# Kernel tuning notes

Measured on AMD Instinct MI355X. Metric: run time of the kernel, lower is better.

The kernel has to match this reference:

```python
import jax, jax.numpy as jnp
import numpy as np

D_FEAT = 64          # d
N_CTX = 8192         # n
N_LAYERS = 4         # l
LMBD = 0.9
DIM = 2 * D_FEAT + 1 # 129


def _decay_matrix(n, lmbd, dtype):
    # M[i, j] = lmbd**(i-j) for j <= i <= n-1 (lower-triangular geometric decay);
    # last row (and hence M[n, n]) is zero, matching the torch loop construction.
    idx = jnp.arange(n + 1)
    diff = idx[:, None] - idx[None, :]
    M = jnp.where(diff >= 0,
                  jnp.power(jnp.asarray(lmbd, dtype), jnp.maximum(diff, 0).astype(dtype)),
                  jnp.zeros((), dtype))
    return M.at[n].set(0.0)


def setup_inputs() -> dict:
    key = jax.random.key(0)
    kz, kp, kq = jax.random.split(key, 3)
    # xavier_normal with gain 0.1 on square (DIM, DIM) weights:
    std = 0.1 * np.sqrt(2.0 / (DIM + DIM))
    Z = jax.random.normal(kz, (DIM, N_CTX + 1), dtype=jnp.float32)
    P = std * jax.random.normal(kp, (DIM, DIM), dtype=jnp.float32)
    Q = std * jax.random.normal(kq, (DIM, DIM), dtype=jnp.float32)
    return {"Z": Z, "P": P, "Q": Q}


def reference(Z, P, Q):
    n = Z.shape[1] - 1
    M = _decay_matrix(n, LMBD, Z.dtype)
    inv_n = jnp.asarray(1.0 / n, Z.dtype)

    def attn(Zc):
        # X = Z^T Q Z : (n+1, n+1)
        X = Zc.T @ Q @ Zc
        A = jax.nn.softmax(X, axis=-1)        # activation('softmax')
        # left-to-right as in torch: ((P @ Z) @ M) @ A, each (DIM, n+1)
        return Zc + inv_n * (((P @ Zc) @ M) @ A)

    for _ in range(N_LAYERS):  # mode='auto': same layer applied l times
        Z = attn(Z)
    return Z
```

## Files before the change

### kernel.cpp

```cpp
#include <hip/hip_runtime.h>

#define D 129
#define N1 8193
#define NN 8192
#define INV_N (1.0f/8192.0f)
#define WSTR 8448
#define KP 160
#define TROWS 8448
#define PSTR 8320

typedef __attribute__((ext_vector_type(8))) short bf16x8;
typedef __attribute__((ext_vector_type(4))) float f32x4;
typedef __attribute__((ext_vector_type(4))) unsigned u32x4;
typedef __attribute__((ext_vector_type(2))) unsigned u32x2;

__device__ __forceinline__ short f2bf(float x){
  unsigned u = __float_as_uint(x);
  unsigned r = (u + 0x7fffu + ((u>>16)&1u)) >> 16;
  return (short)r;
}

__device__ __forceinline__ unsigned cvtpk(float a, float b){
  unsigned r; asm("v_cvt_pk_bf16_f32 %0, %1, %2" : "=v"(r) : "v"(a), "v"(b)); return r;
}

__device__ __forceinline__ float bf2f(unsigned short v){
  return __uint_as_float(((unsigned)v)<<16);
}

#define GLOAD_LDS16(gp, lp) __builtin_amdgcn_global_load_lds( \
    (const __attribute__((address_space(1))) void*)(gp),      \
    (__attribute__((address_space(3))) void*)(lp), 16, 0, 0)

__device__ __forceinline__ int tau(int pos){
  return (pos & 96) + ((pos & 4) << 2) + ((pos & 24) >> 1) + (pos & 3);
}

__global__ void k_tr(const float* __restrict__ src, short* __restrict__ dst, int tmax){
  __shared__ float tile[129][65];
  int t0 = blockIdx.x*64, tid = threadIdx.x;
  for(int idx=tid; idx<129*64; idx+=256){
    int d = idx>>6, c = idx&63;
    tile[d][c] = (t0+c < tmax)? src[(size_t)d*N1 + t0+c] : 0.f;
  }
  __syncthreads();
  int q = tid&3, tl = tid>>2;
  int t = t0 + tl;
  short* row = dst + (size_t)t*KP;
  int s7 = t&7;
  #pragma unroll
  for(int g5=0; g5<5; g5++){
    int gi = q*5 + g5;
    bf16x8 v;
    if(gi < 16){
      #pragma unroll
      for(int u=0;u<8;u++) v[u] = f2bf(tile[gi*8+u][tl]);
      *(bf16x8*)(row + ((gi^s7)<<3)) = v;
    } else if(gi == 16){
      v[0] = f2bf(tile[128][tl]);
      #pragma unroll
      for(int u=1;u<8;u++) v[u] = 0;
      *(bf16x8*)(row + (16<<3)) = v;
    } else {
      #pragma unroll
      for(int u=0;u<8;u++) v[u] = 0;
      *(bf16x8*)(row + (gi<<3)) = v;
    }
  }
}

__global__ __launch_bounds__(512) void k_small(
    const float* __restrict__ Z, const float* __restrict__ P,
    const float* __restrict__ Q, short* __restrict__ YT,
    float* __restrict__ PZ){
  __shared__ float qs[8][132], ps[8][132];
  __shared__ float red[16*256];
  const int tid = threadIdx.x, tx = tid&255, kg = tid>>8;
  const int r0 = blockIdx.y*8;
  for(int i=tid;i<8*129;i+=512){
    int rr=i/129, cc=i-rr*129;
    float qv=0.f, pv=0.f;
    if(r0+rr<D){ qv=Q[(r0+rr)*D+cc]; pv=P[(r0+rr)*D+cc]; }
    qs[rr][cc]=qv; ps[rr][cc]=pv;
  }
  __syncthreads();
  const int t = blockIdx.x*256 + tx;
  const bool valid = (t < N1);
  const int tc = valid ? t : (N1-1);
  const float* zp = Z + tc;
  float ay[8], ap[8];
  #pragma unroll
  for(int rr=0;rr<8;rr++){ ay[rr]=0.f; ap[rr]=0.f; }
  const int kbeg = kg ? 65 : 0, kend = kg ? 129 : 65;
  for(int k=kbeg;k<kend;k++){
    float z = zp[(size_t)k*N1];
    #pragma unroll
    for(int rr=0;rr<8;rr++){
      ay[rr] = fmaf(qs[rr][k], z, ay[rr]);
      ap[rr] = fmaf(ps[rr][k], z, ap[rr]);
    }
  }
  if(kg==1){
    #pragma unroll
    for(int rr=0;rr<8;rr++){
      red[rr*256+tx]     = ay[rr];
      red[(8+rr)*256+tx] = ap[rr];
    }
  }
  __syncthreads();
  if(kg==0){
    #pragma unroll
    for(int rr=0;rr<8;rr++){
      ay[rr] += red[rr*256+tx];
      ap[rr] += red[(8+rr)*256+tx];
    }
    short* row = YT + (size_t)t*KP;
    const int s7 = t&7;
    const int gc = r0>>3;
    bf16x8 v;
    #pragma unroll
    for(int u=0;u<8;u++) v[u] = f2bf(valid ? ay[u] : 0.f);
    if(gc < 16){
      *(bf16x8*)(row + ((gc^s7)<<3)) = v;
    } else {
      *(bf16x8*)(row + (16<<3)) = v;
      bf16x8 zv;
      #pragma unroll
      for(int u=0;u<8;u++) zv[u]=0;
      *(bf16x8*)(row + (17<<3)) = zv;
      *(bf16x8*)(row + (18<<3)) = zv;
      *(bf16x8*)(row + (19<<3)) = zv;
    }
    #pragma unroll
    for(int rr=0;rr<8;rr++){
      int r=r0+rr;
      if(r<D) PZ[(size_t)r*WSTR + t] = valid ? ap[rr] : 0.f;
    }
  }
}

__global__ void k_scan(const float* __restrict__ PZ, float* __restrict__ W){
  __shared__ float s[2376];
  int d = blockIdx.y;
  int base = blockIdx.x*2048;
  for(int i=threadIdx.x;i<2304;i+=128){
    int j = base+i;
    s[i + (i>>5)] = (j<NN)? PZ[(size_t)d*WSTR + j] : 0.f;
  }
  __syncthreads();
  int t = threadIdx.x;
  int jh = t*16+15;
  float acc = 0.f, f = 1.f;
  for(int k=0;k<256;k++){ int a = jh+k; acc = fmaf(f, s[a+(a>>5)], acc); f *= 0.9f; }
  float wv[16];
  wv[15] = acc;
  #pragma unroll
  for(int r=14;r>=0;r--){ int a = t*16+r; wv[r] = fmaf(0.9f, wv[r+1], s[a+(a>>5)]); }
  float* out = W + (size_t)d*WSTR + base + t*16;
  #pragma unroll
  for(int r=0;r<16;r+=4) *(f32x4*)(out+r) = (f32x4){wv[r],wv[r+1],wv[r+2],wv[r+3]};
}

__global__ void k_ssum(const float* __restrict__ S_part, float* __restrict__ S,
                       int i_base, int count){
  int idx = blockIdx.x*256+threadIdx.x;
  if(idx>=count) return;
  int i = i_base + idx;
  float s=0.f;
  #pragma unroll 3
  for(int jtb=0;jtb<33;jtb++) s += S_part[(size_t)jtb*WSTR + i];
  S[i]=s;
}

__global__ void k_v(const float* __restrict__ W, const float* __restrict__ S,
                    short* __restrict__ Vt, int tile0){
  int idx = blockIdx.x*256+threadIdx.x;
  int l = idx/18432, rem = idx - l*18432;
  int d = rem>>7, ci = rem&127;
  int it = tile0 + l;
  int i = it*128 + tau(ci);
  float v = (d<=128)? W[(size_t)d*WSTR + i]/S[i] : 0.f;
  int gs = (ci>>3) ^ (d&7);
  Vt[(size_t)it*18432 + (d<<7) + gs*8 + (ci&7)] = f2bf(v);
}

__global__ __launch_bounds__(512,4) void k_qke(
    const short* __restrict__ ZT, const short* __restrict__ YT,
    short* __restrict__ Ebuf, float* __restrict__ S_part, int tile0, int ITC, int nwg){
  __shared__ short zt[128*KP];
  __shared__ short sp[32*132];
  const int tid=threadIdx.x, w=tid>>6, lane=tid&63, g=lane>>4, lm=lane&15;
  int bid = blockIdx.x;
  int qq = nwg>>3, rr8 = nwg&7, xcd = bid&7, ix = bid>>3;
  int wg = (xcd<rr8 ? xcd*(qq+1) : rr8*(qq+1)+(xcd-rr8)*qq) + ix;
  const int jtb = wg/ITC, itl = wg - jtb*ITC;
  const int it = tile0 + itl;
  const int sx = lm&7;

  const short* ztg = ZT + (size_t)it*(128*KP);
  #pragma unroll
  for(int q=0;q<5;q++){
    int off = (q*512 + tid)*8;
    GLOAD_LDS16(ztg + off, zt + off);
  }

  bf16x8 b[2][5];
  #pragma unroll
  for(int p=0;p<2;p++){
    int jr = jtb*256 + w*32 + p*16 + lm;
    const short* rp = YT + (size_t)jr*KP;
    #pragma unroll
    for(int kk=0;kk<4;kk++) b[p][kk] = *(const bf16x8*)(rp + (((kk*4+g)^sx)<<3));
    b[p][4] = *(const bf16x8*)(rp + ((16+g)<<3));
  }
  const int jl0 = w*32 + lm, jl1 = jl0 + 16;
  const bool jv0 = (jtb*256 + jl0) < N1;
  const bool jv1 = (jtb*256 + jl1) < N1;
  short* ep0 = Ebuf + ((size_t)(jtb*2 + (jl0>>7))*ITC + itl)*16384 + (jl0&127)*128;
  short* ep1 = Ebuf + ((size_t)(jtb*2 + (jl1>>7))*ITC + itl)*16384 + (jl1&127)*128;
  const int wl = w*4 + (lm>>2);
  __syncthreads();

  #pragma unroll
  for(int p2=0;p2<4;p2++){
    const int ib0 = 2*p2, ib1 = ib0+1;
    f32x4 aA0={0.f,0.f,0.f,0.f}, aA1={0.f,0.f,0.f,0.f};
    f32x4 aB0={0.f,0.f,0.f,0.f}, aB1={0.f,0.f,0.f,0.f};
    const short* zpA = zt + (ib0*16+lm)*KP;
    const short* zpB = zt + (ib1*16+lm)*KP;
    #pragma unroll
    for(int kk=0;kk<4;kk++){
      bf16x8 fa = *(const bf16x8*)(zpA + (((kk*4+g)^sx)<<3));
      bf16x8 fb = *(const bf16x8*)(zpB + (((kk*4+g)^sx)<<3));
      aA0 = __builtin_amdgcn_mfma_f32_16x16x32_bf16(fa, b[0][kk], aA0, 0,0,0);
      aA1 = __builtin_amdgcn_mfma_f32_16x16x32_bf16(fa, b[1][kk], aA1, 0,0,0);
      aB0 = __builtin_amdgcn_mfma_f32_16x16x32_bf16(fb, b[0][kk], aB0, 0,0,0);
      aB1 = __builtin_amdgcn_mfma_f32_16x16x32_bf16(fb, b[1][kk], aB1, 0,0,0);
    }
    {
      bf16x8 fa = *(const bf16x8*)(zpA + ((16+g)<<3));
      bf16x8 fb = *(const bf16x8*)(zpB + ((16+g)<<3));
      aA0 = __builtin_amdgcn_mfma_f32_16x16x32_bf16(fa, b[0][4], aA0, 0,0,0);
      aA1 = __builtin_amdgcn_mfma_f32_16x16x32_bf16(fa, b[1][4], aA1, 0,0,0);
      aB0 = __builtin_amdgcn_mfma_f32_16x16x32_bf16(fb, b[0][4], aB0, 0,0,0);
      aB1 = __builtin_amdgcn_mfma_f32_16x16x32_bf16(fb, b[1][4], aB1, 0,0,0);
    }
    float eA0[4], eA1[4], eB0[4], eB1[4];
    #pragma unroll
    for(int r=0;r<4;r++){
      eA0[r] = jv0 ? __expf(aA0[r]) : 0.f;
      eA1[r] = jv1 ? __expf(aA1[r]) : 0.f;
      eB0[r] = jv0 ? __expf(aB0[r]) : 0.f;
      eB1[r] = jv1 ? __expf(aB1[r]) : 0.f;
    }
    const int c0 = p2*4 + g;
    *(u32x4*)(ep0 + (c0<<3)) =
      (u32x4){cvtpk(eA0[0],eA0[1]), cvtpk(eA0[2],eA0[3]), cvtpk(eB0[0],eB0[1]), cvtpk(eB0[2],eB0[3])};
    *(u32x4*)(ep1 + (c0<<3)) =
      (u32x4){cvtpk(eA1[0],eA1[1]), cvtpk(eA1[2],eA1[3]), cvtpk(eB1[0],eB1[1]), cvtpk(eB1[2],eB1[3])};
    float vA[4], vB[4];
    #pragma unroll
    for(int r=0;r<4;r++){
      float sa = eA0[r] + eA1[r];
      sa += __shfl_xor(sa,1); sa += __shfl_xor(sa,2);
      vA[r]=sa;
      float sb = eB0[r] + eB1[r];
      sb += __shfl_xor(sb,1); sb += __shfl_xor(sb,2);
      vB[r]=sb;
    }
    if((lm&3)==0){
      int i0 = p2*32 + g*4;
      *(u32x2*)(sp + wl*132 + i0)      = (u32x2){cvtpk(vA[0],vA[1]), cvtpk(vA[2],vA[3])};
      *(u32x2*)(sp + wl*132 + i0 + 16) = (u32x2){cvtpk(vB[0],vB[1]), cvtpk(vB[2],vB[3])};
    }
  }
  __syncthreads();
  {
    int i = tid>>2, q = tid&3;
    float s=0.f;
    #pragma unroll
    for(int k=0;k<8;k++) s += bf2f((unsigned short)sp[(q*8+k)*132 + i]);
    s += __shfl_xor(s,1); s += __shfl_xor(s,2);
    if(q==0) S_part[(size_t)jtb*WSTR + it*128 + i] = s;
  }
}

__global__ __launch_bounds__(512,4) void k_pv(
    const short* __restrict__ Ebuf, const short* __restrict__ Vt,
    float* __restrict__ part, int ITC, int tile0, int ks_base, int nT){
  __shared__ short vlds[2][18432];
  const int tid=threadIdx.x, w=tid>>6, lane=tid&63, g=lane>>4, lm=lane&15;
  const int jt = blockIdx.x;
  const int ks = ks_base + blockIdx.y;
  const int t0l = blockIdx.y*nT;
  const int sx = lm&7;

  f32x4 acc[9];
  #pragma unroll
  for(int m=0;m<9;m++) acc[m] = (f32x4){0.f,0.f,0.f,0.f};

  auto stageV = [&](int buf, int tl){
    const short* vg = Vt + (size_t)(tile0 + tl)*18432;
    short* vb = &vlds[buf][0];
    #pragma unroll
    for(int q=0;q<5;q++){
      int idx = q*512 + tid;
      if(idx < 2304) GLOAD_LDS16(vg + idx*8, vb + idx*8);
    }
  };
  const short* erow = Ebuf + (size_t)jt*ITC*16384 + (w*16+lm)*128 + (g<<3);
  auto loadE = [&](bf16x8 (&e)[4], int tl){
    const short* ep = erow + (size_t)tl*16384;
    #pragma unroll
    for(int kk=0;kk<4;kk++) e[kk] = *(const bf16x8*)(ep + (kk<<5));
  };
  auto compute = [&](int buf, bf16x8 (&e)[4]){
    const short* vb = &vlds[buf][0];
    #pragma unroll
    for(int kk=0;kk<4;kk++){
      int go = ((kk*4+g)^sx)<<3;
      #pragma unroll
      for(int m=0;m<9;m++){
        bf16x8 av = *(const bf16x8*)(vb + ((m*16+lm)<<7) + go);
        acc[m] = __builtin_amdgcn_mfma_f32_16x16x32_bf16(av, e[kk], acc[m], 0,0,0);
      }
    }
  };

  bf16x8 eA[4], eB[4];
  stageV(0, t0l);
  loadE(eA, t0l);

  for(int t=0; t<nT; t+=2){
    __syncthreads();
    if(t+1<nT){ stageV(1, t0l+t+1); loadE(eB, t0l+t+1); }
    compute(0, eA);
    __syncthreads();
    if(t+2<nT){ stageV(0, t0l+t+2); loadE(eA, t0l+t+2); }
    if(t+1<nT) compute(1, eB);
  }

  float* pb = part + (size_t)ks*144*PSTR;
  const int j = jt*128 + w*16 + lm;
  #pragma unroll
  for(int m=0;m<9;m++){
    #pragma unroll
    for(int r=0;r<4;r++)
      pb[(size_t)(m*16+g*4+r)*PSTR + j] = acc[m][r];
  }
}

__global__ void k_out(const float* __restrict__ Zc, const float* __restrict__ part,
                      float* __restrict__ out, int st){
  int idx = blockIdx.x*256+threadIdx.x;
  if(idx >= 129*2049) return;
  int d = idx/2049, jq = idx - d*2049;
  int j0 = jq*4;
  float s0=0.f,s1=0.f,s2=0.f,s3=0.f;
  for(int ks=0;ks<st;ks++){
    f32x4 v = *(const f32x4*)(part + (size_t)ks*144*PSTR + (size_t)d*PSTR + j0);
    s0+=v[0]; s1+=v[1]; s2+=v[2]; s3+=v[3];
  }
  const float* zr = Zc + (size_t)d*N1;
  float* orow = out + (size_t)d*N1;
  float sv[4] = {s0,s1,s2,s3};
  #pragma unroll
  for(int u=0;u<4;u++){
    int j = j0+u;
    if(j < N1) orow[j] = zr[j] + INV_N*sv[u];
  }
}

extern "C" void kernel_launch(void* const* d_in, const int* in_sizes, int n_in,
                              void* d_out, int out_size, void* d_ws, size_t ws_size,
                              hipStream_t stream){
  (void)in_sizes; (void)n_in; (void)out_size;
  const float* Zin=(const float*)d_in[0];
  const float* Pm =(const float*)d_in[1];
  const float* Qm =(const float*)d_in[2];
  float* out=(float*)d_out;

  const size_t fixed = 2*(size_t)D*N1*4 + 2*(size_t)D*WSTR*4 + (size_t)WSTR*4
                     + (size_t)33*WSTR*4
                     + 2*(size_t)TROWS*KP*2 + (size_t)64*18432*2 + 16*4096;
  int c=8, ksPC=1;
  {
    const int cs[5] = {1,1,2,4,8};
    const int kp[5] = {8,4,2,1,1};
    for(int k=0;k<5;k++){
      int stc = cs[k]*kp[k];
      size_t need = fixed + (size_t)stc*144*PSTR*4 + (size_t)66*(64/cs[k])*16384*2;
      if(need <= ws_size){ c=cs[k]; ksPC=kp[k]; break; }
    }
  }
  const int ITC = 64/c, nT = ITC/ksPC, st = c*ksPC;

  char* base=(char*)d_ws;
  size_t off=0;
  auto alloc=[&](size_t b)->void*{ void* p=base+off; off=(off+b+255)&~(size_t)255; return p; };
  float* Z0  =(float*)alloc((size_t)D*N1*4);
  float* Z1  =(float*)alloc((size_t)D*N1*4);
  float* PZ  =(float*)alloc((size_t)D*WSTR*4);
  float* Wf  =(float*)alloc((size_t)D*WSTR*4);
  float* S   =(float*)alloc((size_t)WSTR*4);
  float* Sp  =(float*)alloc((size_t)33*WSTR*4);
  short* ZT  =(short*)alloc((size_t)TROWS*KP*2);
  short* YT  =(short*)alloc((size_t)TROWS*KP*2);
  short* Vt  =(short*)alloc((size_t)64*18432*2);
  float* part=(float*)alloc((size_t)st*144*PSTR*4);
  short* Ebuf=(short*)alloc((size_t)66*ITC*16384*2);

  const float* Zc=Zin;
  for(int l=0;l<4;l++){
    float* Zn = (l==3)? out : ((l&1)? Z1:Z0);
    k_small<<<dim3(33,17),dim3(512),0,stream>>>(Zc,Pm,Qm,YT,PZ);
    k_tr<<<dim3(132),dim3(256),0,stream>>>(Zc,ZT,N1);
    k_scan<<<dim3(4,D),dim3(128),0,stream>>>(PZ,Wf);
    for(int ch=0; ch<c; ch++){
      int tile0 = ch*ITC;
      int nwg = 33*ITC;
      k_qke<<<dim3(nwg),dim3(512),0,stream>>>(ZT,YT,Ebuf,Sp,tile0,ITC,nwg);
      k_ssum<<<dim3((ITC*128+255)/256),dim3(256),0,stream>>>(Sp,S,tile0*128,ITC*128);
      k_v<<<dim3(ITC*72),dim3(256),0,stream>>>(Wf,S,Vt,tile0);
      k_pv<<<dim3(65,ksPC),dim3(512),0,stream>>>(Ebuf,Vt,part,ITC,tile0,ch*ksPC,nT);
    }
    k_out<<<dim3(1033),dim3(256),0,stream>>>(Zc,part,Zn,st);
    Zc=Zn;
  }
}
```

Before: 626.1 us.

## Store exp scores and V in fp8 and use fp8 MFMA for PV

The exponentiated attention scores (scaled by 1/8) and the normalized V operand (scaled by 4096) are now stored as fp8 instead of bf16. This halves the E buffer and V tile traffic, and the PV product uses the 16x16x32 fp8 MFMA, with the combined scale undone in the output kernel. k_v is rewritten to handle four elements per thread with vector loads and packed fp8 stores. The cost is a large loss of precision in the attention weights and values, which may push the result past the accuracy tolerance.

```diff
diff --git a/kernel.cpp b/kernel.cpp
--- a/kernel.cpp
+++ b/kernel.cpp
@@ -4,6 +4,7 @@
 #define N1 8193
 #define NN 8192
 #define INV_N (1.0f/8192.0f)
+#define OUT_SCALE (1.0f/(8192.0f*512.0f))
 #define WSTR 8448
 #define KP 160
 #define TROWS 8448
@@ -11,8 +12,8 @@
 
 typedef __attribute__((ext_vector_type(8))) short bf16x8;
 typedef __attribute__((ext_vector_type(4))) float f32x4;
-typedef __attribute__((ext_vector_type(4))) unsigned u32x4;
 typedef __attribute__((ext_vector_type(2))) unsigned u32x2;
+typedef long long i64;
 
 __device__ __forceinline__ short f2bf(float x){
   unsigned u = __float_as_uint(x);
@@ -26,6 +27,12 @@
 
 __device__ __forceinline__ float bf2f(unsigned short v){
   return __uint_as_float(((unsigned)v)<<16);
+}
+
+__device__ __forceinline__ int pk_fp8x4(float a, float b, float c, float d){
+  int r = __builtin_amdgcn_cvt_pk_fp8_f32(a, b, 0, false);
+  r = __builtin_amdgcn_cvt_pk_fp8_f32(c, d, r, true);
+  return r;
 }
 
 #define GLOAD_LDS16(gp, lp) __builtin_amdgcn_global_load_lds( \
@@ -173,20 +180,28 @@
 }
 
 __global__ void k_v(const float* __restrict__ W, const float* __restrict__ S,
-                    short* __restrict__ Vt, int tile0){
+                    unsigned char* __restrict__ Vt, int tile0){
   int idx = blockIdx.x*256+threadIdx.x;
-  int l = idx/18432, rem = idx - l*18432;
-  int d = rem>>7, ci = rem&127;
+  int l = idx/4608, rem = idx - l*4608;
+  int d = rem>>5, c4 = rem&31;
+  int ci0 = c4<<2;
   int it = tile0 + l;
-  int i = it*128 + tau(ci);
-  float v = (d<=128)? W[(size_t)d*WSTR + i]/S[i] : 0.f;
-  int gs = (ci>>3) ^ (d&7);
-  Vt[(size_t)it*18432 + (d<<7) + gs*8 + (ci&7)] = f2bf(v);
+  int i0 = it*128 + tau(ci0);
+  float v0=0.f,v1=0.f,v2=0.f,v3=0.f;
+  if(d<=128){
+    f32x4 w4 = *(const f32x4*)(W + (size_t)d*WSTR + i0);
+    f32x4 s4 = *(const f32x4*)(S + i0);
+    v0 = w4[0]/s4[0]*4096.f; v1 = w4[1]/s4[1]*4096.f;
+    v2 = w4[2]/s4[2]*4096.f; v3 = w4[3]/s4[3]*4096.f;
+  }
+  int gs = (ci0>>3) ^ (d&7);
+  int addr = (int)((size_t)0) + (d<<7) + gs*8 + (ci0&7);
+  *(int*)(Vt + (size_t)it*18432 + addr) = pk_fp8x4(v0,v1,v2,v3);
 }
 
 __global__ __launch_bounds__(512,4) void k_qke(
     const short* __restrict__ ZT, const short* __restrict__ YT,
-    short* __restrict__ Ebuf, float* __restrict__ S_part, int tile0, int ITC, int nwg){
+    unsigned char* __restrict__ Ebuf, float* __restrict__ S_part, int tile0, int ITC, int nwg){
   __shared__ short zt[128*KP];
   __shared__ short sp[32*132];
   const int tid=threadIdx.x, w=tid>>6, lane=tid&63, g=lane>>4, lm=lane&15;
@@ -216,8 +231,8 @@
   const int jl0 = w*32 + lm, jl1 = jl0 + 16;
   const bool jv0 = (jtb*256 + jl0) < N1;
   const bool jv1 = (jtb*256 + jl1) < N1;
-  short* ep0 = Ebuf + ((size_t)(jtb*2 + (jl0>>7))*ITC + itl)*16384 + (jl0&127)*128;
-  short* ep1 = Ebuf + ((size_t)(jtb*2 + (jl1>>7))*ITC + itl)*16384 + (jl1&127)*128;
+  unsigned char* ep0 = Ebuf + ((size_t)(jtb*2 + (jl0>>7))*ITC + itl)*16384 + (jl0&127)*128;
+  unsigned char* ep1 = Ebuf + ((size_t)(jtb*2 + (jl1>>7))*ITC + itl)*16384 + (jl1&127)*128;
   const int wl = w*4 + (lm>>2);
   __syncthreads();
 
@@ -254,10 +269,12 @@
       eB1[r] = jv1 ? __expf(aB1[r]) : 0.f;
     }
     const int c0 = p2*4 + g;
-    *(u32x4*)(ep0 + (c0<<3)) =
-      (u32x4){cvtpk(eA0[0],eA0[1]), cvtpk(eA0[2],eA0[3]), cvtpk(eB0[0],eB0[1]), cvtpk(eB0[2],eB0[3])};
-    *(u32x4*)(ep1 + (c0<<3)) =
-      (u32x4){cvtpk(eA1[0],eA1[1]), cvtpk(eA1[2],eA1[3]), cvtpk(eB1[0],eB1[1]), cvtpk(eB1[2],eB1[3])};
+    *(u32x2*)(ep0 + (c0<<3)) = (u32x2){
+      (unsigned)pk_fp8x4(eA0[0]*0.125f, eA0[1]*0.125f, eA0[2]*0.125f, eA0[3]*0.125f),
+      (unsigned)pk_fp8x4(eB0[0]*0.125f, eB0[1]*0.125f, eB0[2]*0.125f, eB0[3]*0.125f)};
+    *(u32x2*)(ep1 + (c0<<3)) = (u32x2){
+      (unsigned)pk_fp8x4(eA1[0]*0.125f, eA1[1]*0.125f, eA1[2]*0.125f, eA1[3]*0.125f),
+      (unsigned)pk_fp8x4(eB1[0]*0.125f, eB1[1]*0.125f, eB1[2]*0.125f, eB1[3]*0.125f)};
     float vA[4], vB[4];
     #pragma unroll
     for(int r=0;r<4;r++){
@@ -286,9 +303,9 @@
 }
 
 __global__ __launch_bounds__(512,4) void k_pv(
-    const short* __restrict__ Ebuf, const short* __restrict__ Vt,
+    const unsigned char* __restrict__ Ebuf, const unsigned char* __restrict__ Vt,
     float* __restrict__ part, int ITC, int tile0, int ks_base, int nT){
-  __shared__ short vlds[2][18432];
+  __shared__ unsigned char vlds[2][18432];
   const int tid=threadIdx.x, w=tid>>6, lane=tid&63, g=lane>>4, lm=lane&15;
   const int jt = blockIdx.x;
   const int ks = ks_base + blockIdx.y;
@@ -300,34 +317,34 @@
   for(int m=0;m<9;m++) acc[m] = (f32x4){0.f,0.f,0.f,0.f};
 
   auto stageV = [&](int buf, int tl){
-    const short* vg = Vt + (size_t)(tile0 + tl)*18432;
-    short* vb = &vlds[buf][0];
-    #pragma unroll
-    for(int q=0;q<5;q++){
+    const unsigned char* vg = Vt + (size_t)(tile0 + tl)*18432;
+    unsigned char* vb = &vlds[buf][0];
+    #pragma unroll
+    for(int q=0;q<3;q++){
       int idx = q*512 + tid;
-      if(idx < 2304) GLOAD_LDS16(vg + idx*8, vb + idx*8);
+      if(idx < 1152) GLOAD_LDS16(vg + idx*16, vb + idx*16);
     }
   };
-  const short* erow = Ebuf + (size_t)jt*ITC*16384 + (w*16+lm)*128 + (g<<3);
-  auto loadE = [&](bf16x8 (&e)[4], int tl){
-    const short* ep = erow + (size_t)tl*16384;
-    #pragma unroll
-    for(int kk=0;kk<4;kk++) e[kk] = *(const bf16x8*)(ep + (kk<<5));
+  const unsigned char* erow = Ebuf + (size_t)jt*ITC*16384 + (w*16+lm)*128 + (g<<3);
+  auto loadE = [&](i64 (&e)[4], int tl){
+    const unsigned char* ep = erow + (size_t)tl*16384;
+    #pragma unroll
+    for(int kk=0;kk<4;kk++) e[kk] = *(const i64*)(ep + (kk<<5));
   };
-  auto compute = [&](int buf, bf16x8 (&e)[4]){
-    const short* vb = &vlds[buf][0];
+  auto compute = [&](int buf, i64 (&e)[4]){
+    const unsigned char* vb = &vlds[buf][0];
     #pragma unroll
     for(int kk=0;kk<4;kk++){
       int go = ((kk*4+g)^sx)<<3;
       #pragma unroll
       for(int m=0;m<9;m++){
-        bf16x8 av = *(const bf16x8*)(vb + ((m*16+lm)<<7) + go);
-        acc[m] = __builtin_amdgcn_mfma_f32_16x16x32_bf16(av, e[kk], acc[m], 0,0,0);
+        i64 av = *(const i64*)(vb + ((m*16+lm)<<7) + go);
+        acc[m] = __builtin_amdgcn_mfma_f32_16x16x32_fp8_fp8(av, e[kk], acc[m], 0,0,0);
       }
     }
   };
 
-  bf16x8 eA[4], eB[4];
+  i64 eA[4], eB[4];
   stageV(0, t0l);
   loadE(eA, t0l);
 
@@ -367,7 +384,7 @@
   #pragma unroll
   for(int u=0;u<4;u++){
     int j = j0+u;
-    if(j < N1) orow[j] = zr[j] + INV_N*sv[u];
+    if(j < N1) orow[j] = zr[j] + OUT_SCALE*sv[u];
   }
 }
 
@@ -382,14 +399,14 @@
 
   const size_t fixed = 2*(size_t)D*N1*4 + 2*(size_t)D*WSTR*4 + (size_t)WSTR*4
                      + (size_t)33*WSTR*4
-                     + 2*(size_t)TROWS*KP*2 + (size_t)64*18432*2 + 16*4096;
+                     + 2*(size_t)TROWS*KP*2 + (size_t)64*18432 + 16*4096;
   int c=8, ksPC=1;
   {
     const int cs[5] = {1,1,2,4,8};
     const int kp[5] = {8,4,2,1,1};
     for(int k=0;k<5;k++){
       int stc = cs[k]*kp[k];
-      size_t need = fixed + (size_t)stc*144*PSTR*4 + (size_t)66*(64/cs[k])*16384*2;
+      size_t need = fixed + (size_t)stc*144*PSTR*4 + (size_t)66*(64/cs[k])*16384;
       if(need <= ws_size){ c=cs[k]; ksPC=kp[k]; break; }
     }
   }
@@ -406,9 +423,9 @@
   float* Sp  =(float*)alloc((size_t)33*WSTR*4);
   short* ZT  =(short*)alloc((size_t)TROWS*KP*2);
   short* YT  =(short*)alloc((size_t)TROWS*KP*2);
-  short* Vt  =(short*)alloc((size_t)64*18432*2);
+  unsigned char* Vt  =(unsigned char*)alloc((size_t)64*18432);
   float* part=(float*)alloc((size_t)st*144*PSTR*4);
-  short* Ebuf=(short*)alloc((size_t)66*ITC*16384*2);
+  unsigned char* Ebuf=(unsigned char*)alloc((size_t)66*ITC*16384);
 
   const float* Zc=Zin;
   for(int l=0;l<4;l++){
@@ -421,7 +438,7 @@
       int nwg = 33*ITC;
       k_qke<<<dim3(nwg),dim3(512),0,stream>>>(ZT,YT,Ebuf,Sp,tile0,ITC,nwg);
       k_ssum<<<dim3((ITC*128+255)/256),dim3(256),0,stream>>>(Sp,S,tile0*128,ITC*128);
-      k_v<<<dim3(ITC*72),dim3(256),0,stream>>>(Wf,S,Vt,tile0);
+      k_v<<<dim3((ITC*4608+255)/256),dim3(256),0,stream>>>(Wf,S,Vt,tile0);
       k_pv<<<dim3(65,ksPC),dim3(512),0,stream>>>(Ebuf,Vt,part,ITC,tile0,ch*ksPC,nT);
     }
     k_out<<<dim3(1033),dim3(256),0,stream>>>(Zc,part,Zn,st);
```

Result: faster. 590.4 us (-5.7%).
